# Performance work log

Hardware: AMD Instinct MI355X
Metric: run time of the kernel (lower is better)

The kernel has to match this reference:

```python
import jax, jax.numpy as jnp
import numpy as np

N, DZ, L, H, MLPH, INC = 256, 256, 256, 512, 2048, 8
CAT_IDX = np.arange(0, 192, 2)                      # 96 categorical token positions (interleaved)
NUM_IDX = np.setdiff1d(np.arange(L), CAT_IDX)       # 160 numerical token positions
CARDS = [4, 16, 128]                                # cardinality per categorical group
GSZ = 32                                            # tokens per categorical group
NUM_CARD = 100                                      # cardinality of quantized numerical params


def setup_inputs() -> dict:
    ks = list(jax.random.split(jax.random.key(0), 24))
    def nrm(shape, s=0.02):
        return jax.random.normal(ks.pop(), shape, jnp.float32) * s
    inp = {}
    inp['z'] = jax.random.normal(ks.pop(), (N, DZ), jnp.float32)
    inp['mlp_w0'] = nrm((DZ, MLPH)); inp['mlp_b0'] = jnp.zeros((MLPH,), jnp.float32)
    inp['mlp_w1'] = nrm((MLPH, MLPH)); inp['mlp_b1'] = jnp.zeros((MLPH,), jnp.float32)
    inp['mlp_w2'] = nrm((MLPH, MLPH)); inp['mlp_b2'] = jnp.zeros((MLPH,), jnp.float32)
    inp['conv_w'] = nrm((H, INC)); inp['conv_b'] = jnp.zeros((H,), jnp.float32)
    for g, card in enumerate(CARDS):
        inp[f'cat_w{g}'] = nrm((H, card)); inp[f'cat_b{g}'] = jnp.zeros((card,), jnp.float32)
    inp['num_w'] = nrm((H, 2)); inp['num_b'] = jnp.zeros((2,), jnp.float32)
    inp['num_target'] = jax.random.uniform(ks.pop(), (N, len(NUM_IDX)), jnp.float32)
    inp['cat_target'] = jax.random.randint(ks.pop(), (N, len(CAT_IDX)), 0, 4, jnp.int32)
    return inp


def reference(z, mlp_w0, mlp_b0, mlp_w1, mlp_b1, mlp_w2, mlp_b2, conv_w, conv_b,
              cat_w0, cat_b0, cat_w1, cat_b1, cat_w2, cat_b2, num_w, num_b,
              num_target, cat_target):
    n = z.shape[0]
    # MLP: fc0 -> act -> fc1 -> act -> fc2
    h = z @ mlp_w0 + mlp_b0
    h = jax.nn.relu(h) @ mlp_w1 + mlp_b1
    h = jax.nn.relu(h) @ mlp_w2 + mlp_b2
    h = h.reshape(n, INC, L)                        # (N, C=8, L)
    # act + 1x1 conv to hidden_size, then transpose -> (N, L, H)
    u = jnp.einsum('ncl,hc->nlh', jax.nn.relu(h), conv_w) + conv_b
    # ---- categorical tokens: gather, per-cardinality heads, CE NLL, argmax sample ----
    hc = u[:, CAT_IDX, :]                           # (N, 96, H)
    heads = [(cat_w0, cat_b0), (cat_w1, cat_b1), (cat_w2, cat_b2)]
    nlls, samps = [], []
    for g, (w, b) in enumerate(heads):
        hg = hc[:, g * GSZ:(g + 1) * GSZ, :]        # (N, 32, H)
        logits = hg @ w + b                         # (N, 32, card)
        logp = jax.nn.log_softmax(logits, axis=-1)
        tg = cat_target[:, g * GSZ:(g + 1) * GSZ]
        nlls.append(-jnp.take_along_axis(logp, tg[..., None], axis=-1)[..., 0])
        samps.append(jnp.argmax(logits, axis=-1))
    cat_nll = jnp.concatenate(nlls, axis=1)         # (N, 96)
    cat_samples = jnp.concatenate(samps, axis=1)    # (N, 96)
    # ---- numerical tokens: gather, 2-param discretized logistic, NLL, mode sample ----
    hn = u[:, NUM_IDX, :]                           # (N, 160, H)
    p = hn @ num_w + num_b                          # (N, 160, 2)
    mu = jax.nn.sigmoid(p[..., 0])
    s = jax.nn.softplus(p[..., 1]) + 1e-4
    hb = 1.0 / (2.0 * (NUM_CARD - 1))               # half bin width
    t = num_target
    cdf_p = jax.nn.sigmoid((t + hb - mu) / s)
    cdf_m = jax.nn.sigmoid((t - hb - mu) / s)
    prob = jnp.where(t < hb, cdf_p, jnp.where(t > 1.0 - hb, 1.0 - cdf_m, cdf_p - cdf_m))
    num_nll = -jnp.log(jnp.maximum(prob, 1e-7))     # (N, 160)
    num_samples = jax.lax.stop_gradient(jnp.round(mu * (NUM_CARD - 1)) / (NUM_CARD - 1))
    # ---- scatter samples back into the preallocated output tensor ----
    u_out = jnp.zeros((n, L, 3), jnp.float32)
    u_out = u_out.at[:, CAT_IDX, 0].set(cat_samples.astype(jnp.float32))
    u_out = u_out.at[:, NUM_IDX, 1].set(num_samples)
    return u_out, cat_nll, num_nll
```

## Files before the change

kernel.cpp:

```cpp
#include <hip/hip_runtime.h>
#include <hip/hip_fp16.h>
#include <math.h>

#define NN   256
#define LL   256
#define HH   512
#define MLPHv 2048
#define INCv 8
#define NCOLS 150

typedef _Float16 f16x8 __attribute__((ext_vector_type(8)));
typedef float    f32x4 __attribute__((ext_vector_type(4)));
typedef unsigned short ushort_t;

__device__ __forceinline__ void split1(float f, ushort_t& h, ushort_t& l)
{
    __half hh = __float2half_rn(f);
    h = __half_as_ushort(hh);
    l = __half_as_ushort(__float2half_rn((f - __half2float(hh)) * 4096.f));
}

__device__ __forceinline__ void pack8(const float* fv, uint4& hv, uint4& lv)
{
    ushort_t h[8], l[8];
#pragma unroll
    for (int j = 0; j < 8; ++j) split1(fv[j], h[j], l[j]);
    hv.x = (unsigned)h[0] | ((unsigned)h[1] << 16);
    hv.y = (unsigned)h[2] | ((unsigned)h[3] << 16);
    hv.z = (unsigned)h[4] | ((unsigned)h[5] << 16);
    hv.w = (unsigned)h[6] | ((unsigned)h[7] << 16);
    lv.x = (unsigned)l[0] | ((unsigned)l[1] << 16);
    lv.y = (unsigned)l[2] | ((unsigned)l[3] << 16);
    lv.z = (unsigned)l[4] | ((unsigned)l[5] << 16);
    lv.w = (unsigned)l[6] | ((unsigned)l[7] << 16);
}

typedef __attribute__((address_space(3))) unsigned int lds_u32;
typedef __attribute__((address_space(1))) const unsigned int glb_u32;
__device__ __forceinline__ void gl_lds16(const ushort_t* g, ushort_t* l)
{
    __builtin_amdgcn_global_load_lds((glb_u32*)g, (lds_u32*)l, 16, 0, 0);
}
__device__ __forceinline__ void gl_lds16f(const float* g, float* l)
{
    __builtin_amdgcn_global_load_lds((glb_u32*)g, (lds_u32*)l, 16, 0, 0);
}


__global__ __launch_bounds__(256) void prep_small(
    const float* __restrict__ z,
    const float* __restrict__ cvw, const float* __restrict__ cvb,
    const float* __restrict__ cw0, const float* __restrict__ cb0,
    const float* __restrict__ cw1, const float* __restrict__ cb1,
    const float* __restrict__ cw2, const float* __restrict__ cb2,
    const float* __restrict__ nw,  const float* __restrict__ nbv,
    ushort_t* __restrict__ zh, ushort_t* __restrict__ zl,
    float* __restrict__ Mf, float* __restrict__ beta)
{
    const int bid = blockIdx.x;
    const int tid = threadIdx.x;
    if (bid < 16) {
        const int idx = bid * 256 + tid;
        const int r = idx >> 4, kq = idx & 15;
        const float* p = z + (size_t)r * 256 + kq * 16;
        float fv[16];
#pragma unroll
        for (int q = 0; q < 4; ++q) {
            float4 v = *(const float4*)(p + q * 4);
            fv[q * 4 + 0] = v.x; fv[q * 4 + 1] = v.y;
            fv[q * 4 + 2] = v.z; fv[q * 4 + 3] = v.w;
        }
        const int gm = r >> 4, l16 = r & 15;
#pragma unroll
        for (int o = 0; o < 2; ++o) {
            uint4 hv, lv;
            pack8(&fv[o * 8], hv, lv);
            const int koct = kq * 2 + o;
            const int ks = koct >> 2, koct3 = koct & 3;
            const size_t off = ((size_t)(gm * 8 + ks) * 64 + l16 + (koct3 << 4)) * 8;
            *(uint4*)&zh[off] = hv;
            *(uint4*)&zl[off] = lv;
        }
    } else {
        const int k = bid - 16;
        const float* W; const float* B; int off, card;
        if (k < 4)        { W = cw0; B = cb0; off = 0;   card = 4;   }
        else if (k < 20)  { W = cw1; B = cb1; off = 4;   card = 16;  }
        else if (k < 148) { W = cw2; B = cb2; off = 20;  card = 128; }
        else              { W = nw;  B = nbv; off = 148; card = 2;   }
        const int kc = k - off;
        float part[INCv + 1];
#pragma unroll
        for (int c = 0; c <= INCv; ++c) part[c] = 0.f;
#pragma unroll
        for (int it = 0; it < 2; ++it) {
            const int h = tid + it * 256;
            const float wv = W[h * card + kc];
#pragma unroll
            for (int c = 0; c < INCv; ++c) part[c] += cvw[h * INCv + c] * wv;
            part[INCv] += cvb[h] * wv;
        }
        __shared__ float red[INCv + 1][4];
        const int lane = tid & 63, wave = tid >> 6;
#pragma unroll
        for (int c = 0; c <= INCv; ++c) {
            float v = part[c];
#pragma unroll
            for (int o = 32; o >= 1; o >>= 1) v += __shfl_down(v, o, 64);
            if (lane == 0) red[c][wave] = v;
        }
        __syncthreads();
        if (tid <= INCv) {
            const float s = red[tid][0] + red[tid][1] + red[tid][2] + red[tid][3];
            if (tid < INCv) Mf[tid * NCOLS + k] = s;
            else            beta[k] = s + B[kc];
        }
    }
}

template <int OUT>
__global__ __launch_bounds__(1024, 1) void gemm_w2(
    const ushort_t* __restrict__ Ah, const ushort_t* __restrict__ Al,
    const float* __restrict__ W, const float* __restrict__ bias,
    float* __restrict__ part, ushort_t* __restrict__ oH, ushort_t* __restrict__ oL,
    int KS32, int kchunk32, int steps)
{
    __shared__ ushort_t sAh[2][8192];
    __shared__ ushort_t sAl[2][8192];
    __shared__ float    sWf[2][4160];
    __shared__ ushort_t sWh[4096];
    __shared__ ushort_t sWl[4096];

    const int tid  = threadIdx.x;
    const int lane = tid & 63, w = tid >> 6;
    const int wr   = w >> 2, wc = w & 3;
    const int bx   = blockIdx.x, by = blockIdx.y, bz = blockIdx.z;
    const int bn   = bx * 64;
    const int kb0  = bz * kchunk32;

    f32x4 accH[2], accC[2];
#pragma unroll
    for (int r = 0; r < 2; ++r) {
        accH[r] = (f32x4){0.f, 0.f, 0.f, 0.f};
        accC[r] = (f32x4){0.f, 0.f, 0.f, 0.f};
    }

    auto STAGE = [&](int ts, int b) {
        const int kb = kb0 + ts * 2;
        const int g = w >> 1, ks = w & 1;
        const size_t fA = ((size_t)(by * 8 + g) * KS32 + kb + ks) * 512 + lane * 8;
        gl_lds16(Ah + fA, &sAh[b][w * 512]);
        gl_lds16(Al + fA, &sAl[b][w * 512]);
        const int k0 = kb * 32;
        const float* src = W + (size_t)(k0 + w * 4 + (lane >> 4)) * 2048 + bn + (lane & 15) * 4;
        gl_lds16f(src, &sWf[b][w * 260]);
    };

    STAGE(0, 0);
    for (int t = 0; t < steps; ++t) {
        const int cur = t & 1;
        if (t + 1 < steps) {
            STAGE(t + 1, cur ^ 1);
            asm volatile("s_waitcnt vmcnt(3)" ::: "memory");
        } else {
            asm volatile("s_waitcnt vmcnt(0)" ::: "memory");
        }
        __builtin_amdgcn_s_barrier();
        asm volatile("" ::: "memory");

        {
            const int col = tid & 63;
            const int q   = tid >> 6;
            const int ks  = q >> 3, koct3 = (q >> 1) & 3, hf = q & 1;
            const int i   = ks * 8 + koct3 * 2 + hf;
            float fv[4];
#pragma unroll
            for (int j = 0; j < 4; ++j) fv[j] = sWf[cur][i * 260 + j * 64 + col];
            ushort_t h[4], l[4];
#pragma unroll
            for (int j = 0; j < 4; ++j) split1(fv[j], h[j], l[j]);
            uint2 hv, lv;
            hv.x = (unsigned)h[0] | ((unsigned)h[1] << 16);
            hv.y = (unsigned)h[2] | ((unsigned)h[3] << 16);
            lv.x = (unsigned)l[0] | ((unsigned)l[1] << 16);
            lv.y = (unsigned)l[2] | ((unsigned)l[3] << 16);
            const int g2 = col >> 4, l16 = col & 15;
            const int ub = ((g2 * 2 + ks) * 64 + l16 + koct3 * 16) * 8 + hf * 4;
            *(uint2*)&sWh[ub] = hv;
            *(uint2*)&sWl[ub] = lv;
        }
        asm volatile("s_waitcnt lgkmcnt(0)" ::: "memory");
        __builtin_amdgcn_s_barrier();
        asm volatile("" ::: "memory");

#pragma unroll
        for (int ks = 0; ks < 2; ++ks) {
            f16x8 aH[2], aL[2], bHf, bLf;
#pragma unroll
            for (int r = 0; r < 2; ++r) {
                const int off = (((wr * 2 + r) * 2 + ks) * 64 + lane) * 8;
                aH[r] = *(const f16x8*)&sAh[cur][off];
                aL[r] = *(const f16x8*)&sAl[cur][off];
            }
            {
                const int off = ((wc * 2 + ks) * 64 + lane) * 8;
                bHf = *(const f16x8*)&sWh[off];
                bLf = *(const f16x8*)&sWl[off];
            }
#pragma unroll
            for (int r = 0; r < 2; ++r) {
                accH[r] = __builtin_amdgcn_mfma_f32_16x16x32_f16(aH[r], bHf, accH[r], 0, 0, 0);
                accC[r] = __builtin_amdgcn_mfma_f32_16x16x32_f16(aH[r], bLf, accC[r], 0, 0, 0);
                accC[r] = __builtin_amdgcn_mfma_f32_16x16x32_f16(aL[r], bHf, accC[r], 0, 0, 0);
            }
        }
        __builtin_amdgcn_s_barrier();
        asm volatile("" ::: "memory");
    }

    const float inv = 1.f / 4096.f;
#pragma unroll
    for (int r = 0; r < 2; ++r) {
        const int row0 = by * 128 + (wr * 2 + r) * 16 + ((lane >> 4) << 2);
        const int col  = bn + wc * 16 + (lane & 15);
        if (OUT == 0) {
            float* po = part + (size_t)bz * 524288;
#pragma unroll
            for (int e = 0; e < 4; ++e)
                po[(size_t)(row0 + e) * 2048 + col] = accH[r][e] + accC[r][e] * inv;
        } else {
            const float vb = bias[col];
            const int gm = by * 8 + wr * 2 + r;
            const int ks = col >> 5, koct3 = (col >> 3) & 3, j = col & 7;
            const size_t fb = ((size_t)(gm * 64 + ks) * 64) * 8 + (koct3 << 4) * 8 + j;
#pragma unroll
            for (int e = 0; e < 4; ++e) {
                const float v = fmaxf(accH[r][e] + accC[r][e] * inv + vb, 0.f);
                ushort_t h, l;
                split1(v, h, l);
                const int l16 = ((lane >> 4) << 2) + e;
                oH[fb + (size_t)l16 * 8] = h;
                oL[fb + (size_t)l16 * 8] = l;
            }
        }
    }
}

__global__ __launch_bounds__(256) void reduce_pk(
    const float* __restrict__ part, const float* __restrict__ bias,
    ushort_t* __restrict__ oH, ushort_t* __restrict__ oL)
{
    const int b  = blockIdx.x;
    const int ct = b & 15, rg = b >> 4;
    const int e  = threadIdx.x * 4;
    const int row = rg * 8 + (e >> 7);
    const int col = ct * 128 + (e & 127);
    const size_t idx = (size_t)row * 2048 + col;
    float4 s = *(const float4*)&bias[col];
#pragma unroll
    for (int k = 0; k < 4; ++k) {
        const float4 p = *(const float4*)&part[(size_t)k * 524288 + idx];
        s.x += p.x; s.y += p.y; s.z += p.z; s.w += p.w;
    }
    s.x = fmaxf(s.x, 0.f); s.y = fmaxf(s.y, 0.f);
    s.z = fmaxf(s.z, 0.f); s.w = fmaxf(s.w, 0.f);
    ushort_t h[4], l[4];
    split1(s.x, h[0], l[0]); split1(s.y, h[1], l[1]);
    split1(s.z, h[2], l[2]); split1(s.w, h[3], l[3]);
    const int gm = row >> 4, l16 = row & 15;
    const int ks = col >> 5, koct3 = (col >> 3) & 3, j = col & 7;
    const size_t off = ((size_t)(gm * 64 + ks) * 64 + l16 + (koct3 << 4)) * 8 + j;
    ushort4 hv = {h[0], h[1], h[2], h[3]};
    ushort4 lv = {l[0], l[1], l[2], l[3]};
    *(ushort4*)&oH[off] = hv;
    *(ushort4*)&oL[off] = lv;
}

__global__ __launch_bounds__(256) void heads_kernel(
    const float* __restrict__ part, const float* __restrict__ b2,
    const float* __restrict__ Mf, const float* __restrict__ beta,
    const int* __restrict__ cat_target, const float* __restrict__ num_target,
    float* __restrict__ out)
{
    const int bx  = blockIdx.x;
    const int tid = threadIdx.x;
    __shared__ float Ms[INCv][128];
    __shared__ float Bsh[128];
    if (bx < 96) {
        const int g = bx >> 5;
        const int card = (g == 0) ? 4 : (g == 1) ? 16 : 128;
        const int off  = (g == 0) ? 0 : (g == 1) ? 4  : 20;
        for (int i = tid; i < card * INCv; i += 256) {
            int c = i / card, k = i % card;
            Ms[c][k] = Mf[c * NCOLS + off + k];
        }
        for (int i = tid; i < card; i += 256) Bsh[i] = beta[off + i];
        __syncthreads();

        const int idx = (bx & 31) * 256 + tid;
        const int n = idx >> 5, j = idx & 31;
        const int ci = g * 32 + j;
        const int l  = ci * 2;
        float rv[INCv];
#pragma unroll
        for (int c = 0; c < INCv; ++c) {
            const size_t e = (size_t)n * MLPHv + c * LL + l;
            float s = b2[c * LL + l];
#pragma unroll
            for (int k = 0; k < 4; ++k) s += part[(size_t)k * 524288 + e];
            rv[c] = fmaxf(s, 0.f);
        }

        float mx = -1e30f; int arg = 0;
        for (int k = 0; k < card; ++k) {
            float s = Bsh[k];
#pragma unroll
            for (int c = 0; c < INCv; ++c) s += rv[c] * Ms[c][k];
            if (s > mx) { mx = s; arg = k; }
        }
        const int tg = cat_target[n * 96 + ci];
        float sum = 0.f, stg = 0.f;
        for (int k = 0; k < card; ++k) {
            float s = Bsh[k];
#pragma unroll
            for (int c = 0; c < INCv; ++c) s += rv[c] * Ms[c][k];
            sum += expf(s - mx);
            if (k == tg) stg = s;
        }
        const float lse = mx + logf(sum);
        out[NN * LL * 3 + n * 96 + ci] = lse - stg;
        float* u = out + (size_t)(n * LL + l) * 3;
        u[0] = (float)arg; u[1] = 0.f; u[2] = 0.f;
    } else {
        const int idx = (bx - 96) * 256 + tid;
        const int n = idx / 160, ni = idx % 160;
        const int l = (ni < 96) ? (2 * ni + 1) : (96 + ni);
        float rv[INCv];
#pragma unroll
        for (int c = 0; c < INCv; ++c) {
            const size_t e = (size_t)n * MLPHv + c * LL + l;
            float s = b2[c * LL + l];
#pragma unroll
            for (int k = 0; k < 4; ++k) s += part[(size_t)k * 524288 + e];
            rv[c] = fmaxf(s, 0.f);
        }
        float p0 = beta[148], p1 = beta[149];
#pragma unroll
        for (int c = 0; c < INCv; ++c) {
            p0 += rv[c] * Mf[c * NCOLS + 148];
            p1 += rv[c] * Mf[c * NCOLS + 149];
        }
        const float mu = 1.f / (1.f + expf(-p0));
        const float sp = (p1 > 20.f) ? p1 : log1pf(expf(p1));
        const float s  = sp + 1e-4f;
        const float hb = 1.f / 198.f;
        const float t  = num_target[n * 160 + ni];
        const float cp = 1.f / (1.f + expf(-((t + hb - mu) / s)));
        const float cm = 1.f / (1.f + expf(-((t - hb - mu) / s)));
        const float prob = (t < hb) ? cp : ((t > 1.f - hb) ? (1.f - cm) : (cp - cm));
        out[NN * LL * 3 + NN * 96 + n * 160 + ni] = -logf(fmaxf(prob, 1e-7f));
        float* u = out + (size_t)(n * LL + l) * 3;
        u[0] = 0.f; u[1] = rintf(mu * 99.f) / 99.f; u[2] = 0.f;
    }
}

extern "C" void kernel_launch(void* const* d_in, const int* in_sizes, int n_in,
                              void* d_out, int out_size, void* d_ws, size_t ws_size,
                              hipStream_t stream)
{
    const float* z   = (const float*)d_in[0];
    const float* w0  = (const float*)d_in[1];
    const float* b0  = (const float*)d_in[2];
    const float* w1  = (const float*)d_in[3];
    const float* b1  = (const float*)d_in[4];
    const float* w2  = (const float*)d_in[5];
    const float* b2  = (const float*)d_in[6];
    const float* cvw = (const float*)d_in[7];
    const float* cvb = (const float*)d_in[8];
    const float* cw0 = (const float*)d_in[9];
    const float* cb0 = (const float*)d_in[10];
    const float* cw1 = (const float*)d_in[11];
    const float* cb1 = (const float*)d_in[12];
    const float* cw2 = (const float*)d_in[13];
    const float* cb2 = (const float*)d_in[14];
    const float* nw  = (const float*)d_in[15];
    const float* nb  = (const float*)d_in[16];
    const float* num_target = (const float*)d_in[17];
    const int*   cat_target = (const int*)d_in[18];
    float* out = (float*)d_out;
    float* ws  = (float*)d_ws;

    size_t o = 0;
    float*    part = ws + o;                o += 4ull * 524288;
    float*    Mf   = ws + o;                o += 1536;
    float*    beta = ws + o;                o += 256;
    ushort_t* zh   = (ushort_t*)(ws + o);   o += 32768;
    ushort_t* zl   = (ushort_t*)(ws + o);   o += 32768;
    ushort_t* r0h  = (ushort_t*)(ws + o);   o += 262144;
    ushort_t* r0l  = (ushort_t*)(ws + o);   o += 262144;
    ushort_t* r1h  = (ushort_t*)(ws + o);   o += 262144;
    ushort_t* r1l  = (ushort_t*)(ws + o);   o += 262144;

    prep_small<<<dim3(166), 256, 0, stream>>>(
        z, cvw, cvb, cw0, cb0, cw1, cb1, cw2, cb2, nw, nb, zh, zl, Mf, beta);

    gemm_w2<1><<<dim3(32, 2, 1), 1024, 0, stream>>>(
        zh, zl, w0, b0, nullptr, r0h, r0l, 8, 8, 4);

    gemm_w2<0><<<dim3(32, 2, 4), 1024, 0, stream>>>(
        r0h, r0l, w1, nullptr, part, nullptr, nullptr, 64, 16, 8);
    reduce_pk<<<dim3(512), 256, 0, stream>>>(part, b1, r1h, r1l);

    gemm_w2<0><<<dim3(32, 2, 4), 1024, 0, stream>>>(
        r1h, r1l, w2, nullptr, part, nullptr, nullptr, 64, 16, 8);

    heads_kernel<<<dim3(256), 256, 0, stream>>>(
        part, b2, Mf, beta, cat_target, num_target, out);
}
```

Before: 72.85 us.

## Halve GEMM M-tile and split fp32 weights to fp16 per-wave in registers

The GEMM kernel now uses 512-thread blocks with a 64-row M tile instead of 1024 threads and 128 rows, doubling the grid along M and allowing two blocks per CU. The shared hi/lo fp16 weight staging buffers and the extra barrier are removed. Each wave now reads the fp32 W tile from LDS and does the fp16 hi/lo split itself in registers before the MFMAs. The aim is to cut LDS use and synchronisation and improve occupancy, at the cost of redundant weight conversion across waves and twice the W global loads per output row.

```diff
diff --git a/kernel.cpp b/kernel.cpp
--- a/kernel.cpp
+++ b/kernel.cpp
@@ -12,6 +12,8 @@
 typedef _Float16 f16x8 __attribute__((ext_vector_type(8)));
 typedef float    f32x4 __attribute__((ext_vector_type(4)));
 typedef unsigned short ushort_t;
+
+union u4f16 { uint4 u; f16x8 v; };
 
 __device__ __forceinline__ void split1(float f, ushort_t& h, ushort_t& l)
 {
@@ -119,17 +121,15 @@
 }
 
 template <int OUT>
-__global__ __launch_bounds__(1024, 1) void gemm_w2(
+__global__ __launch_bounds__(512, 2) void gemm_v3(
     const ushort_t* __restrict__ Ah, const ushort_t* __restrict__ Al,
     const float* __restrict__ W, const float* __restrict__ bias,
     float* __restrict__ part, ushort_t* __restrict__ oH, ushort_t* __restrict__ oL,
     int KS32, int kchunk32, int steps)
 {
-    __shared__ ushort_t sAh[2][8192];
-    __shared__ ushort_t sAl[2][8192];
+    __shared__ ushort_t sAh[2][4096];
+    __shared__ ushort_t sAl[2][4096];
     __shared__ float    sWf[2][4160];
-    __shared__ ushort_t sWh[4096];
-    __shared__ ushort_t sWl[4096];
 
     const int tid  = threadIdx.x;
     const int lane = tid & 63, w = tid >> 6;
@@ -148,12 +148,16 @@
     auto STAGE = [&](int ts, int b) {
         const int kb = kb0 + ts * 2;
         const int g = w >> 1, ks = w & 1;
-        const size_t fA = ((size_t)(by * 8 + g) * KS32 + kb + ks) * 512 + lane * 8;
+        const size_t fA = ((size_t)(by * 4 + g) * KS32 + kb + ks) * 512 + lane * 8;
         gl_lds16(Ah + fA, &sAh[b][w * 512]);
         gl_lds16(Al + fA, &sAl[b][w * 512]);
         const int k0 = kb * 32;
-        const float* src = W + (size_t)(k0 + w * 4 + (lane >> 4)) * 2048 + bn + (lane & 15) * 4;
-        gl_lds16f(src, &sWf[b][w * 260]);
+#pragma unroll
+        for (int ii = 0; ii < 2; ++ii) {
+            const int i = w * 2 + ii;
+            const float* src = W + (size_t)(k0 + i * 4 + (lane >> 4)) * 2048 + bn + (lane & 15) * 4;
+            gl_lds16f(src, &sWf[b][i * 260]);
+        }
     };
 
     STAGE(0, 0);
@@ -161,57 +165,44 @@
         const int cur = t & 1;
         if (t + 1 < steps) {
             STAGE(t + 1, cur ^ 1);
-            asm volatile("s_waitcnt vmcnt(3)" ::: "memory");
+            asm volatile("s_waitcnt vmcnt(4)" ::: "memory");
         } else {
             asm volatile("s_waitcnt vmcnt(0)" ::: "memory");
         }
         __builtin_amdgcn_s_barrier();
         asm volatile("" ::: "memory");
 
-        {
-            const int col = tid & 63;
-            const int q   = tid >> 6;
-            const int ks  = q >> 3, koct3 = (q >> 1) & 3, hf = q & 1;
-            const int i   = ks * 8 + koct3 * 2 + hf;
-            float fv[4];
-#pragma unroll
-            for (int j = 0; j < 4; ++j) fv[j] = sWf[cur][i * 260 + j * 64 + col];
-            ushort_t h[4], l[4];
-#pragma unroll
-            for (int j = 0; j < 4; ++j) split1(fv[j], h[j], l[j]);
-            uint2 hv, lv;
-            hv.x = (unsigned)h[0] | ((unsigned)h[1] << 16);
-            hv.y = (unsigned)h[2] | ((unsigned)h[3] << 16);
-            lv.x = (unsigned)l[0] | ((unsigned)l[1] << 16);
-            lv.y = (unsigned)l[2] | ((unsigned)l[3] << 16);
-            const int g2 = col >> 4, l16 = col & 15;
-            const int ub = ((g2 * 2 + ks) * 64 + l16 + koct3 * 16) * 8 + hf * 4;
-            *(uint2*)&sWh[ub] = hv;
-            *(uint2*)&sWl[ub] = lv;
-        }
-        asm volatile("s_waitcnt lgkmcnt(0)" ::: "memory");
-        __builtin_amdgcn_s_barrier();
-        asm volatile("" ::: "memory");
-
+        f16x8 bH[2], bL[2];
 #pragma unroll
         for (int ks = 0; ks < 2; ++ks) {
-            f16x8 aH[2], aL[2], bHf, bLf;
+            const int col  = wc * 16 + (lane & 15);
+            const int koct = lane >> 4;
+            float fv[8];
+#pragma unroll
+            for (int j = 0; j < 8; ++j) {
+                const int i = ks * 8 + koct * 2 + (j >> 2);
+                fv[j] = sWf[cur][i * 260 + (j & 3) * 64 + col];
+            }
+            u4f16 hv, lv;
+            pack8(fv, hv.u, lv.u);
+            bH[ks] = hv.v;
+            bL[ks] = lv.v;
+        }
+
+#pragma unroll
+        for (int ks = 0; ks < 2; ++ks) {
+            f16x8 aH[2], aL[2];
 #pragma unroll
             for (int r = 0; r < 2; ++r) {
                 const int off = (((wr * 2 + r) * 2 + ks) * 64 + lane) * 8;
                 aH[r] = *(const f16x8*)&sAh[cur][off];
                 aL[r] = *(const f16x8*)&sAl[cur][off];
             }
-            {
-                const int off = ((wc * 2 + ks) * 64 + lane) * 8;
-                bHf = *(const f16x8*)&sWh[off];
-                bLf = *(const f16x8*)&sWl[off];
-            }
 #pragma unroll
             for (int r = 0; r < 2; ++r) {
-                accH[r] = __builtin_amdgcn_mfma_f32_16x16x32_f16(aH[r], bHf, accH[r], 0, 0, 0);
-                accC[r] = __builtin_amdgcn_mfma_f32_16x16x32_f16(aH[r], bLf, accC[r], 0, 0, 0);
-                accC[r] = __builtin_amdgcn_mfma_f32_16x16x32_f16(aL[r], bHf, accC[r], 0, 0, 0);
+                accH[r] = __builtin_amdgcn_mfma_f32_16x16x32_f16(aH[r], bH[ks], accH[r], 0, 0, 0);
+                accC[r] = __builtin_amdgcn_mfma_f32_16x16x32_f16(aH[r], bL[ks], accC[r], 0, 0, 0);
+                accC[r] = __builtin_amdgcn_mfma_f32_16x16x32_f16(aL[r], bH[ks], accC[r], 0, 0, 0);
             }
         }
         __builtin_amdgcn_s_barrier();
@@ -221,7 +212,7 @@
     const float inv = 1.f / 4096.f;
 #pragma unroll
     for (int r = 0; r < 2; ++r) {
-        const int row0 = by * 128 + (wr * 2 + r) * 16 + ((lane >> 4) << 2);
+        const int row0 = by * 64 + (wr * 2 + r) * 16 + ((lane >> 4) << 2);
         const int col  = bn + wc * 16 + (lane & 15);
         if (OUT == 0) {
             float* po = part + (size_t)bz * 524288;
@@ -230,7 +221,7 @@
                 po[(size_t)(row0 + e) * 2048 + col] = accH[r][e] + accC[r][e] * inv;
         } else {
             const float vb = bias[col];
-            const int gm = by * 8 + wr * 2 + r;
+            const int gm = by * 4 + wr * 2 + r;
             const int ks = col >> 5, koct3 = (col >> 3) & 3, j = col & 7;
             const size_t fb = ((size_t)(gm * 64 + ks) * 64) * 8 + (koct3 << 4) * 8 + j;
 #pragma unroll
@@ -404,14 +395,14 @@
     prep_small<<<dim3(166), 256, 0, stream>>>(
         z, cvw, cvb, cw0, cb0, cw1, cb1, cw2, cb2, nw, nb, zh, zl, Mf, beta);
 
-    gemm_w2<1><<<dim3(32, 2, 1), 1024, 0, stream>>>(
+    gemm_v3<1><<<dim3(32, 4, 1), 512, 0, stream>>>(
         zh, zl, w0, b0, nullptr, r0h, r0l, 8, 8, 4);
 
-    gemm_w2<0><<<dim3(32, 2, 4), 1024, 0, stream>>>(
+    gemm_v3<0><<<dim3(32, 4, 4), 512, 0, stream>>>(
         r0h, r0l, w1, nullptr, part, nullptr, nullptr, 64, 16, 8);
     reduce_pk<<<dim3(512), 256, 0, stream>>>(part, b1, r1h, r1l);
 
-    gemm_w2<0><<<dim3(32, 2, 4), 1024, 0, stream>>>(
+    gemm_v3<0><<<dim3(32, 4, 4), 512, 0, stream>>>(
         r1h, r1l, w2, nullptr, part, nullptr, nullptr, 64, 16, 8);
 
     heads_kernel<<<dim3(256), 256, 0, stream>>>(
```

After: 67.48 us (median of 2 runs). -7.4%, faster.
